# Optimization experiments

Measured on AMD Instinct MI355X. Metric: run time of the kernel, lower is better.

## Reference

```python
import jax, jax.numpy as jnp
import numpy as np

N = 100000      # nodes
E = 6400000     # edges (avg degree 64)
S = 8           # FSM states
X = 2 ** S      # neighborhood 'characters' (256)
ITERS = 20      # NeuralFSM.iterations


def setup_inputs() -> dict:
    key = jax.random.key(0)
    k1, k2, k3 = jax.random.split(key, 3)
    # one-hot initial node states [N, S]
    state_idx = jax.random.randint(k1, (N,), 0, S)
    s0 = jax.nn.one_hot(state_idx, S, dtype=jnp.float32)
    # edge list [2, E]
    edge_index = jax.random.randint(k2, (2, E), 0, N, dtype=jnp.int32)
    # FSM transition tensor T[char, state, :] is one-hot over next state -> [X, S, S]
    next_state = jax.random.randint(k3, (X, S), 0, S)
    T = jax.nn.one_hot(next_state, S, dtype=jnp.float32)
    return {"s0": s0, "edge_index": edge_index, "T": T}


def reference(s0, edge_index, T):
    n_nodes, n_states = s0.shape
    src, dst = edge_index[0], edge_index[1]
    powers = (2 ** jnp.arange(n_states)).astype(jnp.int32)  # base-2 encoding of thresholded aggr

    def step(s, _):
        # message = x_j gathered from source nodes, scatter-added at destinations
        msg_sum = jax.ops.segment_sum(s[src], dst, num_segments=n_nodes)  # [N, S]
        # threshold (> 0.5) then clamp to {0,1}
        aggr = (msg_sum > 0.5).astype(jnp.int32)                          # [N, S]
        # multiple-hot -> index into 2^S characters (one-hot folded into a gather)
        idx = aggr @ powers                                               # [N]
        # einsum('x,s,xst->t') with one-hot char == gather T[idx] then contract state
        new_s = jnp.einsum('ns,nst->nt', s, T[idx])                       # [N, S]
        return new_s, None

    s_final, _ = jax.lax.scan(step, s0, None, length=ITERS)
    return s_final
```

## Files before the change

kernel.cpp:

```cpp
#include <hip/hip_runtime.h>
#include <hip/hip_bf16.h>
#include <stdint.h>


#define NN 100000
#define EE 6400000
#define NCHARS 2048
#define ITERS 20

#define NBKT 250
#define NPB 400
#define WPS 12500
#define X4N 3125
#define CEDGE 12800
#define NCHUNK 500
#define CAPB 27648
#define HCAP 13824

#define MEG_TOP     2080
#define CUR_OFF     3328
#define BAR_WORDS   4096

typedef uint32_t u32x4 __attribute__((ext_vector_type(4)));

__device__ inline void mega_barrier(uint32_t* bar, int line, uint32_t epoch) {
    __syncthreads();
    if (threadIdx.x == 0) {
        uint32_t old = atomicAdd(&bar[1664 + line * 16], 1u);
        if (old + 1u == 10u * epoch) {
            uint32_t told = atomicAdd(&bar[MEG_TOP], 1u);
            if (told + 1u == 25u * epoch) {
                for (int r = 0; r < 25; ++r)
                    atomicExch(&bar[2112 + r * 16], epoch);
            }
        }
        while (__hip_atomic_load(&bar[2112 + line * 16], __ATOMIC_RELAXED,
                                 __HIP_MEMORY_SCOPE_AGENT) < epoch)
            __builtin_amdgcn_s_sleep(1);
    }
    __syncthreads();
}

__global__ void __launch_bounds__(512) build_kernel(const int* __restrict__ src,
                                                    const int* __restrict__ dst,
                                                    const float* __restrict__ s0,
                                                    const float* __restrict__ T,
                                                    uint32_t* __restrict__ gPk0,
                                                    uint8_t* __restrict__ nextT,
                                                    uint32_t* __restrict__ csr,
                                                    uint32_t* __restrict__ bar) {
    __shared__ uint32_t stage[CEDGE];
    __shared__ uint32_t cw[8][256];
    __shared__ uint32_t scanb[512];
    __shared__ uint32_t loc[NBKT + 1];
    __shared__ uint32_t segoff[NBKT];
    __shared__ uint8_t  lut[CEDGE];
    int t = threadIdx.x, w = t >> 6;
    int c = blockIdx.x;
    int e0 = c * CEDGE;
    const int4* ps4 = (const int4*)(src + e0);
    const int4* pd4 = (const int4*)(dst + e0);
    uint32_t* cursorG = bar + CUR_OFF;

    if (t < 25) loc[t] = 0;
    __syncthreads();
    if (t < 200) {
        const float* row = s0 + ((size_t)c * 200 + t) * 8;
        int s = 0;
        #pragma unroll
        for (int q = 1; q < 8; ++q) if (row[q] > 0.5f) s = q;
        atomicOr(&loc[t >> 3], (uint32_t)s << ((t & 7) << 2));
    }
    __syncthreads();
    if (t < 25) gPk0[c * 25 + t] = loc[t];
    if (c < 4) {
        const float* row = T + (c * 512 + t) * 8;
        int s = 0;
        #pragma unroll
        for (int q = 1; q < 8; ++q) if (row[q] > 0.5f) s = q;
        nextT[c * 512 + t] = (uint8_t)s;
    }
    __syncthreads();

    for (int i = t; i < 8 * 256; i += 512) ((uint32_t*)cw)[i] = 0;
    __syncthreads();
    for (int i = t; i < CEDGE / 4; i += 512) {
        int4 d = pd4[i];
        atomicAdd(&cw[w][d.x / NPB], 1u);
        atomicAdd(&cw[w][d.y / NPB], 1u);
        atomicAdd(&cw[w][d.z / NPB], 1u);
        atomicAdd(&cw[w][d.w / NPB], 1u);
    }
    __syncthreads();
    uint32_t tot = 0;
    if (t < NBKT) {
        #pragma unroll
        for (int w2 = 0; w2 < 8; ++w2) tot += cw[w2][t];
    }
    scanb[t] = tot;
    __syncthreads();
    for (int off = 1; off < 512; off <<= 1) {
        uint32_t x = (t >= off) ? scanb[t - off] : 0u;
        __syncthreads();
        scanb[t] += x;
        __syncthreads();
    }
    if (t < NBKT) {
        uint32_t excl = scanb[t] - tot;
        loc[t] = excl;
        uint32_t myStart = atomicAdd(&cursorG[t], tot);
        segoff[t] = (uint32_t)t * CAPB + myStart - excl;
        uint32_t acc = excl;
        #pragma unroll
        for (int w2 = 0; w2 < 8; ++w2) {
            uint32_t cv = cw[w2][t];
            cw[w2][t] = acc;
            acc += cv;
        }
    }
    if (t == 0) loc[NBKT] = CEDGE;
    __syncthreads();
    for (int b = t; b < NBKT; b += 512) {
        uint32_t lo = loc[b], hi = loc[b + 1];
        for (uint32_t i = lo; i < hi; ++i) lut[i] = (uint8_t)b;
    }
    for (int i = t; i < CEDGE / 4; i += 512) {
        int4 d = pd4[i];
        int4 s = ps4[i];
        int bb; uint32_t dl, pos;
        bb = d.x / NPB; dl = (uint32_t)(d.x - bb * NPB);
        pos = atomicAdd(&cw[w][bb], 1u);
        stage[pos] = ((uint32_t)(s.x >> 3) << 18) | ((uint32_t)(s.x & 7) << 13) | (dl << 2);
        bb = d.y / NPB; dl = (uint32_t)(d.y - bb * NPB);
        pos = atomicAdd(&cw[w][bb], 1u);
        stage[pos] = ((uint32_t)(s.y >> 3) << 18) | ((uint32_t)(s.y & 7) << 13) | (dl << 2);
        bb = d.z / NPB; dl = (uint32_t)(d.z - bb * NPB);
        pos = atomicAdd(&cw[w][bb], 1u);
        stage[pos] = ((uint32_t)(s.z >> 3) << 18) | ((uint32_t)(s.z & 7) << 13) | (dl << 2);
        bb = d.w / NPB; dl = (uint32_t)(d.w - bb * NPB);
        pos = atomicAdd(&cw[w][bb], 1u);
        stage[pos] = ((uint32_t)(s.w >> 3) << 18) | ((uint32_t)(s.w & 7) << 13) | (dl << 2);
    }
    __syncthreads();
    for (int i = t; i < CEDGE; i += 512) {
        csr[segoff[lut[i]] + (uint32_t)i] = stage[i];
    }
}

__global__ void __launch_bounds__(512) p4_sortsrc(uint32_t* __restrict__ csr,
                                                  const uint32_t* __restrict__ cntG) {
    __shared__ uint32_t st[HCAP];
    __shared__ uint32_t ob[HCAP];
    __shared__ uint32_t binh[512];
    int t = threadIdx.x;
    int j = blockIdx.x;
    int b = j >> 1, h = j & 1;
    uint32_t n  = cntG[b];
    uint32_t n1 = (n + 1) >> 1;
    uint32_t r0 = (uint32_t)b * CAPB + (h ? n1 : 0);
    uint32_t cnt = h ? n - n1 : n1;
    if (cnt > HCAP) return;
    for (uint32_t i = t; i < cnt; i += 512) st[i] = csr[r0 + i];
    binh[t] = 0;
    __syncthreads();
    for (uint32_t i = t; i < cnt; i += 512) atomicAdd(&binh[st[i] >> 23], 1u);
    __syncthreads();
    uint32_t v = binh[t];
    __syncthreads();
    for (int off = 1; off < 512; off <<= 1) {
        uint32_t x = (t >= off) ? binh[t - off] : 0u;
        __syncthreads();
        binh[t] += x;
        __syncthreads();
    }
    uint32_t excl = binh[t] - v;
    __syncthreads();
    binh[t] = excl;
    __syncthreads();
    for (uint32_t i = t; i < cnt; i += 512) {
        uint32_t w = st[i];
        uint32_t pos = atomicAdd(&binh[w >> 23], 1u);
        ob[pos] = w;
    }
    __syncthreads();
    for (uint32_t i = t; i < cnt; i += 512) csr[r0 + i] = ob[i];
}

__global__ void __launch_bounds__(1024) mega_kernel(const uint32_t* __restrict__ csr,
                                                    uint32_t* __restrict__ gPkA,
                                                    uint32_t* __restrict__ gPkB,
                                                    const uint8_t* __restrict__ nextT,
                                                    float* __restrict__ out,
                                                    uint32_t* __restrict__ bar) {
    __shared__ uint32_t sPk[WPS];
    __shared__ uint32_t mask[NPB];
    __shared__ uint32_t packOwn[NPB / 8];
    __shared__ uint8_t  nT[NCHARS];
    __shared__ uint8_t  sown[NPB];
    int t = threadIdx.x;
    int b = blockIdx.x;
    uint32_t base = (uint32_t)b * CAPB;
    uint32_t end  = base + bar[CUR_OFF + b];

    if (t < 512) ((uint32_t*)nT)[t] = ((const uint32_t*)nextT)[t];
    const int line = b % 25;

    for (int p = 0; p < ITERS; ++p) {
        const uint32_t* curG = (p & 1) ? gPkB : gPkA;
        uint32_t*       nxtG = (p & 1) ? gPkA : gPkB;
        {
            const u32x4* g4 = (const u32x4*)curG;
            int i0 = t, i1 = t + 1024, i2 = t + 2048;
            int i3 = t + 3072; if (i3 > X4N - 1) i3 = X4N - 1;
            const u32x4 *p0 = g4 + i0, *p1 = g4 + i1, *p2 = g4 + i2, *p3 = g4 + i3;
            u32x4 a0, a1, a2, a3;
            asm volatile(
                "global_load_dwordx4 %0, %4, off sc1\n\t"
                "global_load_dwordx4 %1, %5, off sc1\n\t"
                "global_load_dwordx4 %2, %6, off sc1\n\t"
                "global_load_dwordx4 %3, %7, off sc1\n\t"
                "s_waitcnt vmcnt(0)"
                : "=&v"(a0), "=&v"(a1), "=&v"(a2), "=&v"(a3)
                : "v"(p0), "v"(p1), "v"(p2), "v"(p3)
                : "memory");
            u32x4* s4 = (u32x4*)sPk;
            s4[i0] = a0; s4[i1] = a1; s4[i2] = a2; s4[i3] = a3;
        }
        if (t < NPB) mask[t] = 0;
        if (t < NPB / 8) packOwn[t] = 0;
        __syncthreads();

        auto edge1 = [&](uint32_t wv) {
            uint32_t val = *(const uint32_t*)((const char*)sPk + (wv >> 16));
            uint32_t nb  = (val >> ((wv >> 11) & 31u)) & 7u;
            atomicOr((uint32_t*)((char*)mask + (wv & 0x7FCu)), 1u << nb);
        };
        uint32_t e = base + ((uint32_t)t << 2);
        for (; e + 4099 < end; e += 8192) {
            u32x4 wa = *(const u32x4*)(csr + e);
            u32x4 wb = *(const u32x4*)(csr + e + 4096);
            edge1(wa.x); edge1(wa.y); edge1(wa.z); edge1(wa.w);
            edge1(wb.x); edge1(wb.y); edge1(wb.z); edge1(wb.w);
        }
        for (; e + 3 < end; e += 4096) {
            u32x4 wa = *(const u32x4*)(csr + e);
            edge1(wa.x); edge1(wa.y); edge1(wa.z); edge1(wa.w);
        }
        for (; e < end; ++e) {
            edge1(csr[e]);
        }
        __syncthreads();

        if (t < NPB) {
            int node = b * NPB + t;
            uint32_t sOwn = (sPk[node >> 3] >> ((node & 7) << 2)) & 7u;
            uint8_t ns = nT[(mask[t] << 3) + sOwn];
            sown[t] = ns;
            atomicOr(&packOwn[t >> 3], (uint32_t)ns << ((t & 7) << 2));
        }
        __syncthreads();
        if (p < ITERS - 1) {
            if (t < NPB / 8)
                __hip_atomic_store(&nxtG[(NPB / 8) * b + t], packOwn[t],
                                   __ATOMIC_RELAXED, __HIP_MEMORY_SCOPE_AGENT);
            mega_barrier(bar, line, (uint32_t)(p + 1));
        }
    }
    __syncthreads();
    for (int f = t; f < NPB * 8; f += 1024) {
        int node = f >> 3;
        out[(size_t)b * (NPB * 8) + f] = ((f & 7) == (int)sown[node]) ? 1.f : 0.f;
    }
}

__global__ void fb_decode(const float* __restrict__ s0, const float* __restrict__ T,
                          uint8_t* __restrict__ state, uint8_t* __restrict__ nextT,
                          uint32_t* __restrict__ mask) {
    int i = blockIdx.x * blockDim.x + threadIdx.x;
    if (i < NCHARS) {
        const float* row = T + i * 8;
        int t = 0;
        #pragma unroll
        for (int k = 1; k < 8; ++k) if (row[k] > 0.5f) t = k;
        nextT[i] = (uint8_t)t;
    }
    if (i < NN) {
        const float* row = s0 + i * 8;
        int s = 0;
        #pragma unroll
        for (int k = 1; k < 8; ++k) if (row[k] > 0.5f) s = k;
        state[i] = (uint8_t)s;
        mask[i] = 0u;
    }
}
__global__ void fb_edge(const int* __restrict__ src, const int* __restrict__ dst,
                        const uint8_t* __restrict__ state, uint32_t* __restrict__ mask) {
    int i = blockIdx.x * blockDim.x + threadIdx.x;
    int stride = gridDim.x * blockDim.x;
    for (int e = i; e < EE; e += stride) atomicOr(&mask[dst[e]], 1u << state[src[e]]);
}
__global__ void fb_update(uint8_t* __restrict__ state, uint32_t* __restrict__ mask,
                          const uint8_t* __restrict__ nextT) {
    int i = blockIdx.x * blockDim.x + threadIdx.x;
    if (i < NN) {
        uint32_t m = mask[i];
        state[i] = nextT[(m << 3) + state[i]];
        mask[i] = 0u;
    }
}
__global__ void fb_output(const uint8_t* __restrict__ state, float* __restrict__ out) {
    int i = blockIdx.x * blockDim.x + threadIdx.x;
    if (i < NN) {
        int s = state[i];
        float4 lo = make_float4(s == 0 ? 1.f : 0.f, s == 1 ? 1.f : 0.f,
                                s == 2 ? 1.f : 0.f, s == 3 ? 1.f : 0.f);
        float4 hi = make_float4(s == 4 ? 1.f : 0.f, s == 5 ? 1.f : 0.f,
                                s == 6 ? 1.f : 0.f, s == 7 ? 1.f : 0.f);
        float4* o = (float4*)(out + (size_t)i * 8);
        o[0] = lo;
        o[1] = hi;
    }
}

extern "C" void kernel_launch(void* const* d_in, const int* in_sizes, int n_in,
                              void* d_out, int out_size, void* d_ws, size_t ws_size,
                              hipStream_t stream) {
    const float* s0  = (const float*)d_in[0];
    const int*   ei  = (const int*)d_in[1];
    const float* T   = (const float*)d_in[2];
    float*       out = (float*)d_out;
    const int* src = ei;
    const int* dst = ei + EE;

    uint8_t* basep = (uint8_t*)d_ws;
    size_t off = 0;
    auto alloc = [&](size_t sz) -> void* {
        void* p = basep + off;
        off += (sz + 255) & ~(size_t)255;
        return p;
    };
    uint32_t* csr   = (uint32_t*)alloc(sizeof(uint32_t) * (size_t)NBKT * CAPB);
    uint8_t*  nextT = (uint8_t*)alloc(NCHARS);
    uint32_t* gPkA  = (uint32_t*)alloc(sizeof(uint32_t) * WPS);
    uint32_t* gPkB  = (uint32_t*)alloc(sizeof(uint32_t) * WPS);
    uint32_t* bar   = (uint32_t*)alloc(sizeof(uint32_t) * BAR_WORDS);
    bool have_ws = (off <= ws_size);

    if (have_ws) {
        hipMemsetAsync(bar, 0, sizeof(uint32_t) * BAR_WORDS, stream);
        build_kernel<<<NCHUNK, 512, 0, stream>>>(src, dst, s0, T, gPkA, nextT, csr, bar);
        p4_sortsrc<<<NBKT * 2, 512, 0, stream>>>(csr, bar + CUR_OFF);
        mega_kernel<<<NBKT, 1024, 0, stream>>>(csr, gPkA, gPkB, nextT, out, bar);
    } else {
        uint32_t* mask = (uint32_t*)d_ws;
        uint8_t*  nT   = (uint8_t*)d_ws + 400128;
        uint8_t*  st   = (uint8_t*)d_ws + 402432;
        fb_decode<<<391, 256, 0, stream>>>(s0, T, st, nT, mask);
        for (int it = 0; it < ITERS; ++it) {
            fb_edge<<<2048, 256, 0, stream>>>(src, dst, st, mask);
            fb_update<<<391, 256, 0, stream>>>(st, mask, nT);
        }
        fb_output<<<391, 256, 0, stream>>>(st, out);
    }
}
```

Baseline: 254.0 us.

## Sort edges by destination and give each thread a contiguous run to coalesce mask atomics

```diff
diff --git a/kernel.cpp b/kernel.cpp
--- a/kernel.cpp
+++ b/kernel.cpp
@@ -156,14 +156,15 @@
     int j = blockIdx.x;
     int b = j >> 1, h = j & 1;
     uint32_t n  = cntG[b];
-    uint32_t n1 = (n + 1) >> 1;
+    uint32_t n1 = (((n + 1) >> 1) + 255u) & ~255u;
+    if (n1 > n) n1 = n;
     uint32_t r0 = (uint32_t)b * CAPB + (h ? n1 : 0);
     uint32_t cnt = h ? n - n1 : n1;
     if (cnt > HCAP) return;
     for (uint32_t i = t; i < cnt; i += 512) st[i] = csr[r0 + i];
     binh[t] = 0;
     __syncthreads();
-    for (uint32_t i = t; i < cnt; i += 512) atomicAdd(&binh[st[i] >> 23], 1u);
+    for (uint32_t i = t; i < cnt; i += 512) atomicAdd(&binh[(st[i] >> 2) & 511u], 1u);
     __syncthreads();
     uint32_t v = binh[t];
     __syncthreads();
@@ -179,7 +180,7 @@
     __syncthreads();
     for (uint32_t i = t; i < cnt; i += 512) {
         uint32_t w = st[i];
-        uint32_t pos = atomicAdd(&binh[w >> 23], 1u);
+        uint32_t pos = atomicAdd(&binh[(w >> 2) & 511u], 1u);
         ob[pos] = w;
     }
     __syncthreads();
@@ -201,6 +202,10 @@
     int b = blockIdx.x;
     uint32_t base = (uint32_t)b * CAPB;
     uint32_t end  = base + bar[CUR_OFF + b];
+    uint32_t cnt  = end - base;
+    uint32_t C  = (((cnt + 1023) >> 10) + 3) & ~3u;
+    uint32_t lo = (uint32_t)t * C;  if (lo > cnt) lo = cnt;
+    uint32_t hi = lo + C;           if (hi > cnt) hi = cnt;
 
     if (t < 512) ((uint32_t*)nT)[t] = ((const uint32_t*)nextT)[t];
     const int line = b % 25;
@@ -230,24 +235,27 @@
         if (t < NPB / 8) packOwn[t] = 0;
         __syncthreads();
 
-        auto edge1 = [&](uint32_t wv) {
-            uint32_t val = *(const uint32_t*)((const char*)sPk + (wv >> 16));
-            uint32_t nb  = (val >> ((wv >> 11) & 31u)) & 7u;
-            atomicOr((uint32_t*)((char*)mask + (wv & 0x7FCu)), 1u << nb);
-        };
-        uint32_t e = base + ((uint32_t)t << 2);
-        for (; e + 4099 < end; e += 8192) {
-            u32x4 wa = *(const u32x4*)(csr + e);
-            u32x4 wb = *(const u32x4*)(csr + e + 4096);
-            edge1(wa.x); edge1(wa.y); edge1(wa.z); edge1(wa.w);
-            edge1(wb.x); edge1(wb.y); edge1(wb.z); edge1(wb.w);
-        }
-        for (; e + 3 < end; e += 4096) {
-            u32x4 wa = *(const u32x4*)(csr + e);
-            edge1(wa.x); edge1(wa.y); edge1(wa.z); edge1(wa.w);
-        }
-        for (; e < end; ++e) {
-            edge1(csr[e]);
+        {
+            uint32_t cur = 0xFFFFFFFFu, acc = 0;
+            auto proc = [&](uint32_t wv) {
+                uint32_t val = *(const uint32_t*)((const char*)sPk + (wv >> 16));
+                uint32_t nb  = (val >> ((wv >> 11) & 31u)) & 7u;
+                uint32_t d   = wv & 0x7FCu;
+                if (d != cur) {
+                    if (cur != 0xFFFFFFFFu)
+                        atomicOr((uint32_t*)((char*)mask + cur), acc);
+                    cur = d; acc = 0;
+                }
+                acc |= 1u << nb;
+            };
+            uint32_t e = base + lo, eh = base + hi;
+            for (; e + 3 < eh; e += 4) {
+                u32x4 wa = *(const u32x4*)(csr + e);
+                proc(wa.x); proc(wa.y); proc(wa.z); proc(wa.w);
+            }
+            for (; e < eh; ++e) proc(csr[e]);
+            if (cur != 0xFFFFFFFFu)
+                atomicOr((uint32_t*)((char*)mask + cur), acc);
         }
         __syncthreads();
 
```

Result: slower. 320.3 us (+26.1%).
